# Kernel optimization log

Measured on AMD Instinct MI355X. Metric: run time of the kernel, lower is better.

Reference implementation:

```python
import jax, jax.numpy as jnp
import numpy as np

MANTISSA_BITS = 8   # mantissa bits incl. sign
BLOCK_SIZE = 16     # elements sharing one exponent


def setup_inputs() -> dict:
    key = jax.random.key(0)
    x = jax.random.normal(key, (4, 4096, 4096), dtype=jnp.float32)
    return {"x": x, "mantissa_bits": MANTISSA_BITS, "block_size": BLOCK_SIZE}


def _bfp_quant(x, mantissa_bits, block_size):
    """Block floating-point quantization: per-block shared exponent + m-bit mantissa."""
    orig_shape = x.shape
    d = orig_shape[-1]
    assert d % block_size == 0
    xb = x.reshape(orig_shape[:-1] + (d // block_size, block_size))
    # shared exponent per block from max magnitude
    max_abs = jnp.max(jnp.abs(xb), axis=-1, keepdims=True)
    safe_max = jnp.where(max_abs > 0, max_abs, jnp.float32(1.0))
    shared_exp = jnp.floor(jnp.log2(safe_max))
    # quantization step: shared_exp scales the m-bit signed mantissa range
    scale = jnp.exp2(shared_exp - (mantissa_bits - 1))
    qmax = jnp.float32(2 ** (mantissa_bits - 1) - 1)
    qmin = jnp.float32(-(2 ** (mantissa_bits - 1)))
    q = jnp.clip(jnp.round(xb / scale), qmin, qmax) * scale
    q = jnp.where(max_abs > 0, q, jnp.zeros_like(q))
    return q.reshape(orig_shape)


def reference(x, mantissa_bits, block_size):
    return _bfp_quant(x, mantissa_bits, block_size)
```

## Files before the change

kernel.cpp:

```cpp
#include <hip/hip_runtime.h>


__global__ __launch_bounds__(256) void bfp_quant_kernel(
    const float4* __restrict__ x, float4* __restrict__ out, int n4) {
    int idx = blockIdx.x * blockDim.x + threadIdx.x;
    if (idx >= n4) return;

    float4 v = x[idx];

    float m = fmaxf(fmaxf(fabsf(v.x), fabsf(v.y)),
                    fmaxf(fabsf(v.z), fabsf(v.w)));
    m = fmaxf(m, __shfl_xor(m, 1));
    m = fmaxf(m, __shfl_xor(m, 2));

    float sm = (m > 0.0f) ? m : 1.0f;

    int e = (int)(__float_as_uint(sm) >> 23) - 127;

    float scale = ldexpf(1.0f, e - 7);
    float inv   = ldexpf(1.0f, 7 - e);

    float4 q;
    q.x = fminf(fmaxf(rintf(v.x * inv), -128.0f), 127.0f) * scale;
    q.y = fminf(fmaxf(rintf(v.y * inv), -128.0f), 127.0f) * scale;
    q.z = fminf(fmaxf(rintf(v.z * inv), -128.0f), 127.0f) * scale;
    q.w = fminf(fmaxf(rintf(v.w * inv), -128.0f), 127.0f) * scale;

    out[idx] = q;
}

extern "C" void kernel_launch(void* const* d_in, const int* in_sizes, int n_in,
                              void* d_out, int out_size, void* d_ws, size_t ws_size,
                              hipStream_t stream) {
    const float* x = (const float*)d_in[0];
    float* out = (float*)d_out;
    int n = in_sizes[0];
    int n4 = n >> 2;

    const int threads = 256;
    int blocks = (n4 + threads - 1) / threads;
    bfp_quant_kernel<<<blocks, threads, 0, stream>>>(
        (const float4*)x, (float4*)out, n4);
}
```

Measured before the change: 416.3 us.

## Process one 16-element block per thread with nontemporal stores

Each thread now loads four float4 vectors covering a full quantization block and computes the block max locally, removing the cross-lane shuffles. Outputs are written with nontemporal stores to avoid polluting caches, and ldexp uses the AMDGCN builtin. The per-lane access stride becomes 64 bytes, which may reduce coalescing efficiency per load instruction, and there are four times fewer threads.

Result: slower. 546.8 us (+31.3%).

```diff
diff --git a/kernel.cpp b/kernel.cpp
--- a/kernel.cpp
+++ b/kernel.cpp
@@ -1,32 +1,44 @@
 #include <hip/hip_runtime.h>
 
 
+typedef float vfloat4 __attribute__((ext_vector_type(4)));
+
 __global__ __launch_bounds__(256) void bfp_quant_kernel(
-    const float4* __restrict__ x, float4* __restrict__ out, int n4) {
-    int idx = blockIdx.x * blockDim.x + threadIdx.x;
-    if (idx >= n4) return;
+    const vfloat4* __restrict__ x, vfloat4* __restrict__ out, int nblk) {
+    int b = blockIdx.x * blockDim.x + threadIdx.x;
+    if (b >= nblk) return;
 
-    float4 v = x[idx];
+    const vfloat4* px = x + (size_t)b * 4;
+    vfloat4 v0 = px[0];
+    vfloat4 v1 = px[1];
+    vfloat4 v2 = px[2];
+    vfloat4 v3 = px[3];
 
-    float m = fmaxf(fmaxf(fabsf(v.x), fabsf(v.y)),
-                    fmaxf(fabsf(v.z), fabsf(v.w)));
-    m = fmaxf(m, __shfl_xor(m, 1));
-    m = fmaxf(m, __shfl_xor(m, 2));
+    float m0 = fmaxf(fmaxf(fabsf(v0.x), fabsf(v0.y)), fmaxf(fabsf(v0.z), fabsf(v0.w)));
+    float m1 = fmaxf(fmaxf(fabsf(v1.x), fabsf(v1.y)), fmaxf(fabsf(v1.z), fabsf(v1.w)));
+    float m2 = fmaxf(fmaxf(fabsf(v2.x), fabsf(v2.y)), fmaxf(fabsf(v2.z), fabsf(v2.w)));
+    float m3 = fmaxf(fmaxf(fabsf(v3.x), fabsf(v3.y)), fmaxf(fabsf(v3.z), fabsf(v3.w)));
+    float m = fmaxf(fmaxf(m0, m1), fmaxf(m2, m3));
 
     float sm = (m > 0.0f) ? m : 1.0f;
 
     int e = (int)(__float_as_uint(sm) >> 23) - 127;
 
-    float scale = ldexpf(1.0f, e - 7);
-    float inv   = ldexpf(1.0f, 7 - e);
+    float scale = __builtin_amdgcn_ldexpf(1.0f, e - 7);
+    float inv   = __builtin_amdgcn_ldexpf(1.0f, 7 - e);
 
-    float4 q;
-    q.x = fminf(fmaxf(rintf(v.x * inv), -128.0f), 127.0f) * scale;
-    q.y = fminf(fmaxf(rintf(v.y * inv), -128.0f), 127.0f) * scale;
-    q.z = fminf(fmaxf(rintf(v.z * inv), -128.0f), 127.0f) * scale;
-    q.w = fminf(fmaxf(rintf(v.w * inv), -128.0f), 127.0f) * scale;
+#define QQ(t) (fminf(fmaxf(rintf((t) * inv), -128.0f), 127.0f) * scale)
+    vfloat4 q0 = {QQ(v0.x), QQ(v0.y), QQ(v0.z), QQ(v0.w)};
+    vfloat4 q1 = {QQ(v1.x), QQ(v1.y), QQ(v1.z), QQ(v1.w)};
+    vfloat4 q2 = {QQ(v2.x), QQ(v2.y), QQ(v2.z), QQ(v2.w)};
+    vfloat4 q3 = {QQ(v3.x), QQ(v3.y), QQ(v3.z), QQ(v3.w)};
+#undef QQ
 
-    out[idx] = q;
+    vfloat4* po = out + (size_t)b * 4;
+    __builtin_nontemporal_store(q0, po + 0);
+    __builtin_nontemporal_store(q1, po + 1);
+    __builtin_nontemporal_store(q2, po + 2);
+    __builtin_nontemporal_store(q3, po + 3);
 }
 
 extern "C" void kernel_launch(void* const* d_in, const int* in_sizes, int n_in,
@@ -35,10 +47,10 @@
     const float* x = (const float*)d_in[0];
     float* out = (float*)d_out;
     int n = in_sizes[0];
-    int n4 = n >> 2;
+    int nblk = n >> 4;
 
     const int threads = 256;
-    int blocks = (n4 + threads - 1) / threads;
+    int blocks = (nblk + threads - 1) / threads;
     bfp_quant_kernel<<<blocks, threads, 0, stream>>>(
-        (const float4*)x, (float4*)out, n4);
+        (const vfloat4*)x, (vfloat4*)out, nblk);
 }
```
